# Optimization experiments

Hardware: AMD Instinct MI355X
Metric: run time of the kernel (lower is better)

## Reference

```python
import jax, jax.numpy as jnp
import numpy as np

N_HEADS = 16


def setup_inputs() -> dict:
    key = jax.random.key(0)
    k1, k2, k3 = jax.random.split(key, 3)
    n_embed = 1024
    b, t = 4, 2048
    x = jax.random.normal(k1, (b, t, n_embed), dtype=jnp.float32)
    # Linear weights stored as [in, out]; y = x @ W + b (same math as torch Linear).
    Wqkv = jax.random.normal(k2, (n_embed, 3 * n_embed), dtype=jnp.float32) * (n_embed ** -0.5)
    bqkv = jnp.zeros((3 * n_embed,), dtype=jnp.float32)
    Wout = jax.random.normal(k3, (n_embed, n_embed), dtype=jnp.float32) * (n_embed ** -0.5)
    bout = jnp.zeros((n_embed,), dtype=jnp.float32)
    return {"x": x, "Wqkv": Wqkv, "bqkv": bqkv, "Wout": Wout, "bout": bout}


def reference(x, Wqkv, bqkv, Wout, bout):
    b, t, n_embed = x.shape
    hs = n_embed // N_HEADS
    qkv = x @ Wqkv + bqkv  # [b, t, 3*n_embed]
    q, k, v = jnp.split(qkv, 3, axis=-1)
    # b t (h hs) -> b h t hs
    def to_heads(u):
        return u.reshape(b, t, N_HEADS, hs).transpose(0, 2, 1, 3)
    q, k, v = to_heads(q), to_heads(k), to_heads(v)
    scale = 1.0 / jnp.sqrt(jnp.asarray(hs, dtype=x.dtype))
    scores = jnp.einsum('bhqd,bhkd->bhqk', q, k) * scale  # [b, h, t, t]
    causal = jnp.tril(jnp.ones((t, t), dtype=bool))
    scores = jnp.where(causal, scores, jnp.finfo(scores.dtype).min)
    attn = jax.nn.softmax(scores, axis=-1)
    out = jnp.einsum('bhqk,bhkd->bhqd', attn, v)  # [b, h, t, hs]
    out = out.transpose(0, 2, 1, 3).reshape(b, t, n_embed)  # b h t hs -> b t (h hs)
    return out @ Wout + bout
```

## Files before the change

### kernel.cpp

```cpp
#include <hip/hip_runtime.h>
#include <hip/hip_bf16.h>
#include <stdint.h>

typedef unsigned short u16;
typedef __bf16 bf16x8 __attribute__((ext_vector_type(8)));
typedef float f32x4 __attribute__((ext_vector_type(4)));
typedef u16 ushort8 __attribute__((ext_vector_type(8)));
typedef short short4v __attribute__((ext_vector_type(4)));

__device__ __forceinline__ u16 f2bf(float f) {
    unsigned int u = __builtin_bit_cast(unsigned int, f);
    u += 0x7fffu + ((u >> 16) & 1u);
    return (u16)(u >> 16);
}

__device__ __forceinline__ unsigned pk2(float a, float b) {
    __hip_bfloat162 h = __float22bfloat162_rn(float2{a, b});
    unsigned u;
    __builtin_memcpy(&u, &h, 4);
    return u;
}

#define MFMA16(a, b, c) __builtin_amdgcn_mfma_f32_16x16x32_bf16( \
    __builtin_bit_cast(bf16x8, a), __builtin_bit_cast(bf16x8, b), c, 0, 0, 0)

#if defined(__has_builtin)
#if __has_builtin(__builtin_amdgcn_exp2f)
#define EXP2(x) __builtin_amdgcn_exp2f(x)
#endif
#endif
#ifndef EXP2
#define EXP2(x) __expf((x) * 0.69314718f)
#endif

__device__ __forceinline__ void async16(void* lds, const void* g) {
    __builtin_amdgcn_global_load_lds(
        (const __attribute__((address_space(1))) unsigned int*)(uintptr_t)g,
        (__attribute__((address_space(3))) unsigned int*)(unsigned int)(uintptr_t)lds,
        16, 0, 0);
}

__device__ __forceinline__ void transpose_tile(
    const float* __restrict__ src, u16* __restrict__ dst,
    int N, int K, int k0, int n0, int tid, u16* T)
{
    const int rr = tid >> 4, cc = (tid & 15) * 4;
    #pragma unroll
    for (int rnd = 0; rnd < 4; ++rnd) {
        int r = rr + rnd * 16;
        float4 f = *(const float4*)&src[(size_t)(k0 + r) * N + n0 + cc];
        u16 v[4] = {f2bf(f.x), f2bf(f.y), f2bf(f.z), f2bf(f.w)};
        *(unsigned long long*)&T[r * 68 + cc] = *(unsigned long long*)v;
    }
    __syncthreads();
    #pragma unroll
    for (int rnd = 0; rnd < 4; ++rnd) {
        int rn = rr + rnd * 16;
        u16 v[4];
        #pragma unroll
        for (int j = 0; j < 4; ++j) v[j] = T[(cc + j) * 68 + rn];
        *(unsigned long long*)&dst[(size_t)(n0 + rn) * K + k0 + cc] =
            *(unsigned long long*)v;
    }
}

__global__ __launch_bounds__(256) void prep_kernel(
    const float* __restrict__ x, u16* __restrict__ xb,
    const float* __restrict__ Wqkv, u16* __restrict__ wT)
{
    __shared__ u16 T[64 * 68];
    const int blk = blockIdx.x, tid = threadIdx.x;
    if (blk < 4096) {
        int i = blk * 256 + tid;
        float4 f0 = ((const float4*)x)[i * 2];
        float4 f1 = ((const float4*)x)[i * 2 + 1];
        ushort8 v;
        v[0]=f2bf(f0.x); v[1]=f2bf(f0.y); v[2]=f2bf(f0.z); v[3]=f2bf(f0.w);
        v[4]=f2bf(f1.x); v[5]=f2bf(f1.y); v[6]=f2bf(f1.z); v[7]=f2bf(f1.w);
        ((ushort8*)xb)[i] = v;
    } else {
        int idx = blk - 4096;
        int k0 = (idx & 15) * 64, n0 = (idx >> 4) * 64;
        transpose_tile(Wqkv, wT, 3072, 1024, k0, n0, tid, T);
    }
}

#define NT32 32
#define BUF32 16384

__device__ __forceinline__ void stage32(
    const u16* __restrict__ A, const u16* __restrict__ Bt,
    u16* Lb, int m0, int n0, int k0, int w, int lane)
{
    const int rbl = lane >> 5;
    const int chunk = (lane >> 3) & 3;
    const int row = lane & 7;
    #pragma unroll
    for (int r = 0; r < 2; ++r) {
        int rb = w * 4 + r * 2 + rbl;
        async16(Lb + (w * 4 + r * 2) * 256,
                A + (size_t)(m0 + rb * 8 + row) * 1024 + k0 + chunk * 8);
    }
    #pragma unroll
    for (int r = 0; r < 2; ++r) {
        int rb = w * 4 + r * 2 + rbl;
        async16(Lb + 8192 + (w * 4 + r * 2) * 256,
                Bt + (size_t)(n0 + rb * 8 + row) * 1024 + k0 + chunk * 8);
    }
}

__device__ __forceinline__ void gemm_mainloop32(
    const u16* __restrict__ A, const u16* __restrict__ Bt,
    u16* L, int m0, int n0, int tid, f32x4 acc[8][4])
{
    const int lane = tid & 63, w = tid >> 6;
    const int lr = lane & 15, quad = lane >> 4;
    const int wm = w >> 2, wn = w & 3;
    const int arb = wm * 16 + (lr >> 3);
    const int brb = wn * 8 + (lr >> 3);
    const int foff = quad * 64 + (lr & 7) * 8;

    stage32(A, Bt, L, m0, n0, 0, w, lane);
    asm volatile("s_waitcnt vmcnt(0)" ::: "memory");
    __builtin_amdgcn_s_barrier();
    asm volatile("" ::: "memory");

    #pragma unroll 2
    for (int t = 0; t < NT32; ++t) {
        const u16* As = L + (t & 1) * BUF32;
        const u16* Bs = As + 8192;

        if (t + 1 < NT32) {
            stage32(A, Bt, L + ((t + 1) & 1) * BUF32, m0, n0, (t + 1) * 32,
                    w, lane);
            asm volatile("s_waitcnt vmcnt(4)" ::: "memory");
        } else {
            asm volatile("s_waitcnt vmcnt(0)" ::: "memory");
        }
        __builtin_amdgcn_s_barrier();
        asm volatile("" ::: "memory");

        ushort8 b[4], a03[4], a47[4];
        #pragma unroll
        for (int nt = 0; nt < 4; ++nt)
            b[nt] = *(const ushort8*)&Bs[(brb + nt * 2) * 256 + foff];
        #pragma unroll
        for (int mt = 0; mt < 4; ++mt)
            a03[mt] = *(const ushort8*)&As[(arb + mt * 2) * 256 + foff];
        __builtin_amdgcn_sched_barrier(0);
        #pragma unroll
        for (int mt = 0; mt < 4; ++mt)
            a47[mt] = *(const ushort8*)&As[(arb + (mt + 4) * 2) * 256 + foff];
        asm volatile("s_waitcnt lgkmcnt(4)" ::: "memory");
        __builtin_amdgcn_sched_barrier(0);
        __builtin_amdgcn_s_setprio(1);
        #pragma unroll
        for (int mt = 0; mt < 4; ++mt)
            #pragma unroll
            for (int nt = 0; nt < 4; ++nt)
                acc[mt][nt] = MFMA16(a03[mt], b[nt], acc[mt][nt]);
        __builtin_amdgcn_s_setprio(0);
        asm volatile("s_waitcnt lgkmcnt(0)" ::: "memory");
        __builtin_amdgcn_sched_barrier(0);
        __builtin_amdgcn_s_setprio(1);
        #pragma unroll
        for (int mt = 0; mt < 4; ++mt)
            #pragma unroll
            for (int nt = 0; nt < 4; ++nt)
                acc[mt + 4][nt] = MFMA16(a47[mt], b[nt], acc[mt + 4][nt]);
        __builtin_amdgcn_s_setprio(0);
        __builtin_amdgcn_s_barrier();
        asm volatile("" ::: "memory");
    }
}

__global__ __launch_bounds__(512, 2) void qkv_gemm(
    const u16* __restrict__ xb, const u16* __restrict__ Wt,
    const float* __restrict__ bias, u16* __restrict__ qkvb)
{
    __shared__ u16 L[2 * BUF32];
    const int m0 = blockIdx.x * 256, n0 = blockIdx.y * 256;
    const int tid = threadIdx.x;
    f32x4 acc[8][4] = {};
    gemm_mainloop32(xb, Wt, L, m0, n0, tid, acc);

    const int lane = tid & 63, w = tid >> 6;
    const int lr = lane & 15, quad = lane >> 4;
    const int wm = w >> 2, wn = w & 3;
    const int which = n0 >> 10;
    float bv[4];
    #pragma unroll
    for (int nt = 0; nt < 4; ++nt) bv[nt] = bias[n0 + wn * 64 + nt * 16 + lr];

    if (which == 2) {
        u16* vT = qkvb + (size_t)2 * 8388608;
        #pragma unroll
        for (int nt = 0; nt < 4; ++nt) {
            int n = n0 + wn * 64 + nt * 16 + lr;
            int hh = (n >> 6) & 15, d = n & 63;
            #pragma unroll
            for (int mt = 0; mt < 8; ++mt) {
                int mbase = m0 + wm * 128 + mt * 16 + quad * 4;
                int b_idx = mbase >> 11, t0 = mbase & 2047;
                short4v o4;
                #pragma unroll
                for (int reg = 0; reg < 4; ++reg)
                    o4[reg] = (short)f2bf(acc[mt][nt][reg] + bv[nt]);
                *(short4v*)&vT[((size_t)(b_idx * 16 + hh) * 64 + d) * 2048 + t0] = o4;
            }
        }
    } else {
        u16* dst = qkvb + (size_t)which * 8388608;
        #pragma unroll
        for (int mt = 0; mt < 8; ++mt)
          #pragma unroll
          for (int nt = 0; nt < 4; ++nt) {
            int n = n0 + wn * 64 + nt * 16 + lr;
            int hh = (n >> 6) & 15, d = n & 63;
            #pragma unroll
            for (int reg = 0; reg < 4; ++reg) {
                int m = m0 + wm * 128 + mt * 16 + quad * 4 + reg;
                int b_idx = m >> 11, t_idx = m & 2047;
                dst[(((size_t)(b_idx * 16 + hh) * 2048 + t_idx) << 6) + d] =
                    f2bf(acc[mt][nt][reg] + bv[nt]);
            }
          }
    }
}

#define KT16 16

__device__ __forceinline__ void stage_tile256(
    const u16* __restrict__ A, const u16* __restrict__ Bt,
    u16* Lb, int m0, int n0, int k0, int w, int grow, int gchunk)
{
    #pragma unroll
    for (int r = 0; r < 4; ++r) {
        int rb = w * 4 + r;
        async16(Lb + rb * 512,
                A + (size_t)(m0 + rb * 8 + grow) * 1024 + k0 + gchunk * 8);
    }
    #pragma unroll
    for (int r = 0; r < 2; ++r) {
        int rb = w * 2 + r;
        async16(Lb + 16384 + rb * 512,
                Bt + (size_t)(n0 + rb * 8 + grow) * 1024 + k0 + gchunk * 8);
    }
}

__device__ __forceinline__ void gemm_mainloop256(
    const u16* __restrict__ A, const u16* __restrict__ Bt,
    u16* L, int m0, int n0, int tid, f32x4 acc[4][4])
{
    const int lane = tid & 63, w = tid >> 6;
    const int lr = lane & 15, quad = lane >> 4;
    const int wm = w >> 1, wn = w & 1;
    const int grow = lane & 7, gchunk = lane >> 3;

    stage_tile256(A, Bt, L,         m0, n0, 0,  w, grow, gchunk);
    stage_tile256(A, Bt, L + 24576, m0, n0, 64, w, grow, gchunk);

    u16* Lc = L;
    u16* Ls = L + 49152;
    u16* const Lend = L + 73728;

    for (int t = 0; t < KT16; ++t) {
        if (t < KT16 - 2)
            stage_tile256(A, Bt, Ls, m0, n0, (t + 2) * 64, w, grow, gchunk);

        if (t < KT16 - 2)       asm volatile("s_waitcnt vmcnt(12)" ::: "memory");
        else if (t == KT16 - 2) asm volatile("s_waitcnt vmcnt(6)"  ::: "memory");
        else                    asm volatile("s_waitcnt vmcnt(0)"  ::: "memory");
        __builtin_amdgcn_s_barrier();
        asm volatile("" ::: "memory");

        const u16* As = Lc;
        const u16* Bs = Lc + 16384;
        __builtin_amdgcn_s_setprio(1);
        #pragma unroll
        for (int kk = 0; kk < 2; ++kk) {
            ushort8 a[4], b[4];
            #pragma unroll
            for (int mt = 0; mt < 4; ++mt) {
                int rb = wm * 8 + mt * 2 + (lr >> 3);
                a[mt] = *(const ushort8*)&As[rb * 512 + (kk * 4 + quad) * 64 + (lr & 7) * 8];
            }
            #pragma unroll
            for (int nt = 0; nt < 4; ++nt) {
                int rb = wn * 8 + nt * 2 + (lr >> 3);
                b[nt] = *(const ushort8*)&Bs[rb * 512 + (kk * 4 + quad) * 64 + (lr & 7) * 8];
            }
            #pragma unroll
            for (int mt = 0; mt < 4; ++mt)
                #pragma unroll
                for (int nt = 0; nt < 4; ++nt)
                    acc[mt][nt] = MFMA16(a[mt], b[nt], acc[mt][nt]);
        }
        __builtin_amdgcn_s_setprio(0);
        asm volatile("" ::: "memory");
        __builtin_amdgcn_s_barrier();
        asm volatile("" ::: "memory");

        Lc += 24576; if (Lc == Lend) Lc = L;
        Ls += 24576; if (Ls == Lend) Ls = L;
    }
}

__global__ __launch_bounds__(512, 2) void out_gemm(
    const u16* __restrict__ A, const u16* __restrict__ Wt,
    const float* __restrict__ bias, float* __restrict__ out)
{
    __shared__ u16 L[73728];
    const int m0 = blockIdx.x * 256, n0 = blockIdx.y * 128;
    const int tid = threadIdx.x;
    f32x4 acc[4][4] = {};
    gemm_mainloop256(A, Wt, L, m0, n0, tid, acc);

    const int lane = tid & 63, w = tid >> 6;
    const int lr = lane & 15, quad = lane >> 4;
    const int wm = w >> 1, wn = w & 1;
    float bv[4];
    #pragma unroll
    for (int nt = 0; nt < 4; ++nt) bv[nt] = bias[n0 + wn * 64 + nt * 16 + lr];
    #pragma unroll
    for (int mt = 0; mt < 4; ++mt)
      #pragma unroll
      for (int nt = 0; nt < 4; ++nt)
        #pragma unroll
        for (int reg = 0; reg < 4; ++reg) {
            int m = m0 + wm * 64 + mt * 16 + quad * 4 + reg;
            int n = n0 + wn * 64 + nt * 16 + lr;
            out[(size_t)m * 1024 + n] = acc[mt][nt][reg] + bv[nt];
        }
}

__global__ __launch_bounds__(256) void attn_kernel(
    const u16* __restrict__ qkvb, u16* __restrict__ o_ws,
    const float* __restrict__ Wout, u16* __restrict__ wT)
{
    __shared__ u16 SH[16896];
    const int tid = threadIdx.x;

    if (blockIdx.z == 4) {
        int idx = blockIdx.x + 16 * blockIdx.y;
        int k0 = (idx & 15) * 64, n0 = (idx >> 4) * 64;
        transpose_tile(Wout, wT, 1024, 1024, k0, n0, tid, SH);
        return;
    }

    u16* Ks0 = SH;
    u16* Vts = SH + 8192;
    u16* Ps  = SH + 12288;

    const int orig = blockIdx.x + 16 * (blockIdx.y + 16 * blockIdx.z);
    const int work = (orig & 7) * 128 + (orig >> 3);
    const int p = work & 15, h = (work >> 4) & 15, b = work >> 8;
    const size_t bh = (size_t)(b * 16 + h) * 131072;
    const u16* Qb = qkvb + bh;
    const u16* Kb = qkvb + 8388608 + bh;
    const u16* Vt = qkvb + 2 * 8388608 + bh;
    const int lane = tid & 63, w = tid >> 6;
    const int lr = lane & 15, quad = lane >> 4;
    const int grow = lane & 7, gchunk = lane >> 3;
    const float kscale = 0.125f * 1.44269504f;

    for (int pass = 0; pass < 2; ++pass) {
        const int qt = pass ? (31 - p) : p;
        ushort8 qf[2];
        {
            const u16* qr = Qb + (size_t)(qt * 64 + w * 16 + lr) * 64 + quad * 8;
            qf[0] = *(const ushort8*)qr;
            qf[1] = *(const ushort8*)(qr + 32);
        }
        f32x4 o_acc[4] = {};
        float m_i = -1e30f, l_i = 0.f;
        const int qrow = w * 16 + lr;
        const int bsrc = (lane & 48) + ((lane >> 4) << 2);

        __syncthreads();
        #pragma unroll
        for (int r = 0; r < 2; ++r) {
            int rb = w * 2 + r;
            async16(&Ks0[rb * 512], Kb + (size_t)(rb * 8 + grow) * 64 + gchunk * 8);
        }

        for (int kt = 0; kt <= qt; ++kt) {
            const int buf = kt & 1;
            __syncthreads();

            #pragma unroll
            for (int r = 0; r < 2; ++r) {
                int rb = w * 2 + r;
                if (kt < qt)
                    async16(&Ks0[(buf ^ 1) * 4096 + rb * 512],
                            Kb + (size_t)((kt + 1) * 64 + rb * 8 + grow) * 64 + gchunk * 8);
                async16(&Vts[rb * 512],
                        Vt + (size_t)(rb * 8 + grow) * 2048 + kt * 64 + gchunk * 8);
            }

            f32x4 s[4] = {};
            #pragma unroll
            for (int nt = 0; nt < 4; ++nt)
                #pragma unroll
                for (int kk = 0; kk < 2; ++kk) {
                    ushort8 bb = *(ushort8*)&Ks0[buf * 4096 +
                                                 (nt * 2 + (lr >> 3)) * 512 +
                                                 (kk * 4 + quad) * 64 + (lr & 7) * 8];
                    s[nt] = MFMA16(bb, qf[kk], s[nt]);
                }
            if (kt == qt) {
                #pragma unroll
                for (int nt = 0; nt < 4; ++nt)
                    #pragma unroll
                    for (int reg = 0; reg < 4; ++reg) {
                        int kc = nt * 16 + quad * 4 + reg;
                        if (kc > qrow) s[nt][reg] = -1e30f;
                    }
            }
            float mx = -1e30f;
            #pragma unroll
            for (int nt = 0; nt < 4; ++nt)
                #pragma unroll
                for (int reg = 0; reg < 4; ++reg) mx = fmaxf(mx, s[nt][reg]);
            mx = fmaxf(mx, __shfl_xor(mx, 16, 64));
            mx = fmaxf(mx, __shfl_xor(mx, 32, 64));
            float mxs = mx * kscale;
            if (!__all(mxs <= m_i + 8.0f)) {
                float mnew = fmaxf(m_i, mxs);
                float alpha = EXP2(m_i - mnew);
                m_i = mnew;
                l_i *= alpha;
                #pragma unroll
                for (int reg = 0; reg < 4; ++reg) {
                    float ar = __shfl(alpha, bsrc + reg, 64);
                    #pragma unroll
                    for (int dt = 0; dt < 4; ++dt) o_acc[dt][reg] *= ar;
                }
            }
            float p4[4][4];
            float rs = 0.f;
            #pragma unroll
            for (int nt = 0; nt < 4; ++nt)
                #pragma unroll
                for (int reg = 0; reg < 4; ++reg) {
                    float pv = EXP2(fmaf(s[nt][reg], kscale, -m_i));
                    p4[nt][reg] = pv;
                    rs += pv;
                }
            rs += __shfl_xor(rs, 16, 64);
            rs += __shfl_xor(rs, 32, 64);
            l_i += rs;
            #pragma unroll
            for (int nt = 0; nt < 4; ++nt) {
                unsigned lo = pk2(p4[nt][0], p4[nt][1]);
                unsigned hi = pk2(p4[nt][2], p4[nt][3]);
                unsigned long long pk = ((unsigned long long)hi << 32) | lo;
                *(unsigned long long*)&Ps[qrow * 72 + nt * 16 + quad * 4] = pk;
            }

            __syncthreads();

            #pragma unroll
            for (int kk = 0; kk < 2; ++kk) {
                ushort8 pa = *(ushort8*)&Ps[(w * 16 + lr) * 72 + kk * 32 + quad * 8];
                #pragma unroll
                for (int dt = 0; dt < 4; ++dt) {
                    ushort8 vb = *(ushort8*)&Vts[(dt * 2 + (lr >> 3)) * 512 +
                                                 (kk * 4 + quad) * 64 + (lr & 7) * 8];
                    o_acc[dt] = MFMA16(pa, vb, o_acc[dt]);
                }
            }
        }

        float rinv = 1.0f / l_i;
        float rl[4];
        #pragma unroll
        for (int reg = 0; reg < 4; ++reg) rl[reg] = __shfl(rinv, bsrc + reg, 64);
        #pragma unroll
        for (int dt = 0; dt < 4; ++dt)
            #pragma unroll
            for (int reg = 0; reg < 4; ++reg) {
                int row = w * 16 + quad * 4 + reg;
                int tq = qt * 64 + row;
                o_ws[((size_t)(b * 2048 + tq) << 10) + h * 64 + dt * 16 + lr] =
                    f2bf(o_acc[dt][reg] * rl[reg]);
            }
    }
}

extern "C" void kernel_launch(void* const* d_in, const int* in_sizes, int n_in,
                              void* d_out, int out_size, void* d_ws, size_t ws_size,
                              hipStream_t stream)
{
    const float* x    = (const float*)d_in[0];
    const float* Wqkv = (const float*)d_in[1];
    const float* bqkv = (const float*)d_in[2];
    const float* Wout = (const float*)d_in[3];
    const float* bout = (const float*)d_in[4];
    float* out = (float*)d_out;

    u16* qkvb = (u16*)d_ws;
    u16* xb   = qkvb + (size_t)3 * 8388608;
    u16* wT   = qkvb + (size_t)4 * 8388608;
    u16* attn_o = xb;

    prep_kernel<<<4864, 256, 0, stream>>>(x, xb, Wqkv, wT);
    qkv_gemm<<<dim3(32, 12), 512, 0, stream>>>(xb, wT, bqkv, qkvb);
    attn_kernel<<<dim3(16, 16, 5), 256, 0, stream>>>(qkvb, attn_o, Wout, wT);
    out_gemm<<<dim3(32, 8), 512, 0, stream>>>(attn_o, wT, bout, out);
}
```

Baseline: 268.2 us.

## Shrink out-projection GEMM to 128x128 tiles with double-buffered K=32 staging

Rewrites the output projection GEMM to use 128x128 block tiles with 256 threads and a K-step of 32, double-buffered in a much smaller LDS footprint, replacing the 256x128, 512-thread, triple-buffered K=64 mainloop. The grid doubles to 512 blocks to fill more CUs and raise occupancy for this small GEMM. The trade is twice as many K iterations, each with barriers, and lower data reuse per block. The new loop depends on an NT32 constant assumed to be defined in the hidden part of the file.

Result: slower. 274.0 us (median of 2 runs) (+2.2%).

```diff
diff --git a/kernel.cpp b/kernel.cpp
--- a/kernel.cpp
+++ b/kernel.cpp
@@ -228,97 +228,84 @@
     }
 }
 
-#define KT16 16
-
-__device__ __forceinline__ void stage_tile256(
+#define OBUF 8192
+
+__device__ __forceinline__ void stage128(
     const u16* __restrict__ A, const u16* __restrict__ Bt,
-    u16* Lb, int m0, int n0, int k0, int w, int grow, int gchunk)
-{
-    #pragma unroll
-    for (int r = 0; r < 4; ++r) {
-        int rb = w * 4 + r;
-        async16(Lb + rb * 512,
-                A + (size_t)(m0 + rb * 8 + grow) * 1024 + k0 + gchunk * 8);
-    }
+    u16* Lb, int m0, int n0, int k0, int w, int lane)
+{
+    const int rbl = lane >> 5;
+    const int chunk = (lane >> 3) & 3;
+    const int row = lane & 7;
     #pragma unroll
     for (int r = 0; r < 2; ++r) {
-        int rb = w * 2 + r;
-        async16(Lb + 16384 + rb * 512,
-                Bt + (size_t)(n0 + rb * 8 + grow) * 1024 + k0 + gchunk * 8);
-    }
-}
-
-__device__ __forceinline__ void gemm_mainloop256(
-    const u16* __restrict__ A, const u16* __restrict__ Bt,
-    u16* L, int m0, int n0, int tid, f32x4 acc[4][4])
-{
+        int pb = w * 2 + r;
+        async16(Lb + pb * 512,
+                A + (size_t)(m0 + pb * 16 + rbl * 8 + row) * 1024 + k0 + chunk * 8);
+    }
+    #pragma unroll
+    for (int r = 0; r < 2; ++r) {
+        int pb = w * 2 + r;
+        async16(Lb + 4096 + pb * 512,
+                Bt + (size_t)(n0 + pb * 16 + rbl * 8 + row) * 1024 + k0 + chunk * 8);
+    }
+}
+
+__global__ __launch_bounds__(256) void out_gemm(
+    const u16* __restrict__ A, const u16* __restrict__ Wt,
+    const float* __restrict__ bias, float* __restrict__ out)
+{
+    __shared__ u16 L[2 * OBUF];
+    const int m0 = blockIdx.x * 128, n0 = blockIdx.y * 128;
+    const int tid = threadIdx.x;
     const int lane = tid & 63, w = tid >> 6;
     const int lr = lane & 15, quad = lane >> 4;
     const int wm = w >> 1, wn = w & 1;
-    const int grow = lane & 7, gchunk = lane >> 3;
-
-    stage_tile256(A, Bt, L,         m0, n0, 0,  w, grow, gchunk);
-    stage_tile256(A, Bt, L + 24576, m0, n0, 64, w, grow, gchunk);
-
-    u16* Lc = L;
-    u16* Ls = L + 49152;
-    u16* const Lend = L + 73728;
-
-    for (int t = 0; t < KT16; ++t) {
-        if (t < KT16 - 2)
-            stage_tile256(A, Bt, Ls, m0, n0, (t + 2) * 64, w, grow, gchunk);
-
-        if (t < KT16 - 2)       asm volatile("s_waitcnt vmcnt(12)" ::: "memory");
-        else if (t == KT16 - 2) asm volatile("s_waitcnt vmcnt(6)"  ::: "memory");
-        else                    asm volatile("s_waitcnt vmcnt(0)"  ::: "memory");
+    const int arb = wm * 8 + (lr >> 3);
+    const int brb = wn * 8 + (lr >> 3);
+    const int foff = quad * 64 + (lr & 7) * 8;
+    f32x4 acc[4][4] = {};
+
+    stage128(A, Wt, L, m0, n0, 0, w, lane);
+    asm volatile("s_waitcnt vmcnt(0)" ::: "memory");
+    __builtin_amdgcn_s_barrier();
+    asm volatile("" ::: "memory");
+
+    #pragma unroll 2
+    for (int t = 0; t < NT32; ++t) {
+        const u16* As = L + (t & 1) * OBUF;
+        const u16* Bs = As + 4096;
+
+        if (t + 1 < NT32) {
+            stage128(A, Wt, L + ((t + 1) & 1) * OBUF, m0, n0, (t + 1) * 32,
+                     w, lane);
+            asm volatile("s_waitcnt vmcnt(4)" ::: "memory");
+        } else {
+            asm volatile("s_waitcnt vmcnt(0)" ::: "memory");
+        }
         __builtin_amdgcn_s_barrier();
         asm volatile("" ::: "memory");
 
-        const u16* As = Lc;
-        const u16* Bs = Lc + 16384;
+        ushort8 b[4], a[4];
+        #pragma unroll
+        for (int nt = 0; nt < 4; ++nt)
+            b[nt] = *(const ushort8*)&Bs[(brb + nt * 2) * 256 + foff];
+        #pragma unroll
+        for (int mt = 0; mt < 4; ++mt)
+            a[mt] = *(const ushort8*)&As[(arb + mt * 2) * 256 + foff];
+        asm volatile("s_waitcnt lgkmcnt(0)" ::: "memory");
+        __builtin_amdgcn_sched_barrier(0);
         __builtin_amdgcn_s_setprio(1);
         #pragma unroll
-        for (int kk = 0; kk < 2; ++kk) {
-            ushort8 a[4], b[4];
-            #pragma unroll
-            for (int mt = 0; mt < 4; ++mt) {
-                int rb = wm * 8 + mt * 2 + (lr >> 3);
-                a[mt] = *(const ushort8*)&As[rb * 512 + (kk * 4 + quad) * 64 + (lr & 7) * 8];
-            }
-            #pragma unroll
-            for (int nt = 0; nt < 4; ++nt) {
-                int rb = wn * 8 + nt * 2 + (lr >> 3);
-                b[nt] = *(const ushort8*)&Bs[rb * 512 + (kk * 4 + quad) * 64 + (lr & 7) * 8];
-            }
-            #pragma unroll
-            for (int mt = 0; mt < 4; ++mt)
-                #pragma unroll
-                for (int nt = 0; nt < 4; ++nt)
-                    acc[mt][nt] = MFMA16(a[mt], b[nt], acc[mt][nt]);
-        }
+        for (int mt = 0; mt < 4; ++mt)
+            #pragma unroll
+            for (int nt = 0; nt < 4; ++nt)
+                acc[mt][nt] = MFMA16(a[mt], b[nt], acc[mt][nt]);
         __builtin_amdgcn_s_setprio(0);
-        asm volatile("" ::: "memory");
         __builtin_amdgcn_s_barrier();
         asm volatile("" ::: "memory");
-
-        Lc += 24576; if (Lc == Lend) Lc = L;
-        Ls += 24576; if (Ls == Lend) Ls = L;
-    }
-}
-
-__global__ __launch_bounds__(512, 2) void out_gemm(
-    const u16* __restrict__ A, const u16* __restrict__ Wt,
-    const float* __restrict__ bias, float* __restrict__ out)
-{
-    __shared__ u16 L[73728];
-    const int m0 = blockIdx.x * 256, n0 = blockIdx.y * 128;
-    const int tid = threadIdx.x;
-    f32x4 acc[4][4] = {};
-    gemm_mainloop256(A, Wt, L, m0, n0, tid, acc);
-
-    const int lane = tid & 63, w = tid >> 6;
-    const int lr = lane & 15, quad = lane >> 4;
-    const int wm = w >> 1, wn = w & 1;
+    }
+
     float bv[4];
     #pragma unroll
     for (int nt = 0; nt < 4; ++nt) bv[nt] = bias[n0 + wn * 64 + nt * 16 + lr];
@@ -507,5 +494,5 @@
     prep_kernel<<<4864, 256, 0, stream>>>(x, xb, Wqkv, wT);
     qkv_gemm<<<dim3(32, 12), 512, 0, stream>>>(xb, wT, bqkv, qkvb);
     attn_kernel<<<dim3(16, 16, 5), 256, 0, stream>>>(qkvb, attn_o, Wout, wT);
-    out_gemm<<<dim3(32, 8), 512, 0, stream>>>(attn_o, wT, bout, out);
-}
+    out_gemm<<<dim3(64, 8), 256, 0, stream>>>(attn_o, wT, bout, out);
+}
```
